# Performance work log

Measured on AMD Instinct MI355X. Metric: run time of the kernel, lower is better.

## Reference

```python
import jax, jax.numpy as jnp
import numpy as np

TAU = 1.0
MAX_ITER = 10


def setup_inputs() -> dict:
    key = jax.random.key(0)
    s = jax.random.normal(key, (32, 1024, 1024), dtype=jnp.float32)
    return {"s": s}


def reference(s) -> jnp.ndarray:
    # s: [B, N1, N2] with N1 <= N2 (square here), no padding -> fully vectorized
    log_s = s / TAU
    for i in range(MAX_ITER):
        # even iter: row normalization (logsumexp over columns, axis=2)
        # odd  iter: column normalization (logsumexp over rows, axis=1)
        axis = 2 if i % 2 == 0 else 1
        log_s = log_s - jax.nn.logsumexp(log_s, axis=axis, keepdims=True)
    return jnp.exp(log_s)
```

## Files before the change

### kernel.cpp

```cpp
#include <hip/hip_runtime.h>
#include <math.h>


#define BATCH 32
#define N 1024
#define RCHUNKS 32
#define ROWS_PER_BLK 32
#define BGROUPS 2
#define ROWS_PER_GROUP 16
#define PCHUNKS RCHUNKS

__global__ __launch_bounds__(512, 4) void fused_pair_kernel(
    const float* __restrict__ s, const float* __restrict__ c,
    float* __restrict__ r, float* __restrict__ pm, float* __restrict__ pl,
    int has_c)
{
    const int bc    = blockIdx.x;
    const int b     = bc >> 5;
    const int chunk = bc & 31;
    const int row0  = chunk * ROWS_PER_BLK;

    __shared__ float cs[N];
    __shared__ float rs[ROWS_PER_BLK];
    __shared__ float sm[BGROUPS][N];
    __shared__ float sl[BGROUPS][N];

    if (has_c) {
        ((float2*)cs)[threadIdx.x] = ((const float2*)(c + b * N))[threadIdx.x];
    } else {
        ((float2*)cs)[threadIdx.x] = make_float2(0.f, 0.f);
    }
    __syncthreads();

    const int wave = threadIdx.x >> 6;
    const int lane = threadIdx.x & 63;
    const float4* cs4 = (const float4*)cs;
#pragma unroll
    for (int rp = 0; rp < 4; rp++) {
        const int row = wave * 4 + rp;
        const float4* srow = (const float4*)(s + ((size_t)(b * N + row0 + row)) * N);
        float x[16];
#pragma unroll
        for (int k = 0; k < 4; k++) {
            float4 v  = srow[lane + 64 * k];
            float4 cv = cs4[lane + 64 * k];
            x[4*k+0] = v.x + cv.x; x[4*k+1] = v.y + cv.y;
            x[4*k+2] = v.z + cv.z; x[4*k+3] = v.w + cv.w;
        }
        float m = x[0];
#pragma unroll
        for (int t = 1; t < 16; t++) m = fmaxf(m, x[t]);
#pragma unroll
        for (int off = 32; off > 0; off >>= 1) m = fmaxf(m, __shfl_xor(m, off, 64));
        float sum = 0.f;
#pragma unroll
        for (int t = 0; t < 16; t++) sum += __expf(x[t] - m);
#pragma unroll
        for (int off = 32; off > 0; off >>= 1) sum += __shfl_xor(sum, off, 64);
        if (lane == 0) {
            float rv = -(m + __logf(sum));
            rs[row] = rv;
            r[b * N + row0 + row] = rv;
        }
    }
    __syncthreads();

    const int j4 = threadIdx.x & 255;
    const int g  = threadIdx.x >> 8;
    const float4* sb4 = (const float4*)(s + ((size_t)(b * N + row0 + g * ROWS_PER_GROUP)) * N);
    float m0=-3.0e38f, m1=-3.0e38f, m2=-3.0e38f, m3=-3.0e38f;
    float l0=0.f, l1=0.f, l2=0.f, l3=0.f;
#pragma unroll
    for (int i = 0; i < ROWS_PER_GROUP; i++) {
        float ri = rs[g * ROWS_PER_GROUP + i];
        float4 v = sb4[(size_t)i * 256 + j4];
        float x0 = v.x + ri, x1 = v.y + ri, x2 = v.z + ri, x3 = v.w + ri;
        float n0 = fmaxf(m0, x0); l0 = l0 * __expf(m0 - n0) + __expf(x0 - n0); m0 = n0;
        float n1 = fmaxf(m1, x1); l1 = l1 * __expf(m1 - n1) + __expf(x1 - n1); m1 = n1;
        float n2 = fmaxf(m2, x2); l2 = l2 * __expf(m2 - n2) + __expf(x2 - n2); m2 = n2;
        float n3 = fmaxf(m3, x3); l3 = l3 * __expf(m3 - n3) + __expf(x3 - n3); m3 = n3;
    }
    ((float4*)sm[g])[j4] = make_float4(m0, m1, m2, m3);
    ((float4*)sl[g])[j4] = make_float4(l0, l1, l2, l3);
    __syncthreads();

#pragma unroll
    for (int cc = 0; cc < 2; cc++) {
        const int col = threadIdx.x + cc * 512;
        float M = sm[0][col], L = sl[0][col];
        float m = sm[1][col], l = sl[1][col];
        float mn = fmaxf(M, m);
        L = L * __expf(M - mn) + l * __expf(m - mn);
        pm[(size_t)bc * N + col] = mn;
        pl[(size_t)bc * N + col] = L;
    }
}

__global__ __launch_bounds__(1024) void col_combine_kernel(
    const float* __restrict__ pm, const float* __restrict__ pl,
    float* __restrict__ c)
{
    const int b  = blockIdx.x >> 2;
    const int q  = blockIdx.x & 3;
    const int jc = threadIdx.x & 255;
    const int kg = threadIdx.x >> 8;
    const int j  = q * 256 + jc;
    float M = -3.0e38f, L = 0.f;
#pragma unroll
    for (int k = 0; k < 8; k++) {
        const int kk = kg * 8 + k;
        float m = pm[((size_t)(b * PCHUNKS + kk)) * N + j];
        float l = pl[((size_t)(b * PCHUNKS + kk)) * N + j];
        float mn = fmaxf(M, m);
        L = L * __expf(M - mn) + l * __expf(m - mn); M = mn;
    }
    __shared__ float smm[4][256], sll[4][256];
    smm[kg][jc] = M; sll[kg][jc] = L;
    __syncthreads();
    if (kg == 0) {
#pragma unroll
        for (int g2 = 1; g2 < 4; g2++) {
            float m = smm[g2][jc], l = sll[g2][jc];
            float mn = fmaxf(M, m);
            L = L * __expf(M - mn) + l * __expf(m - mn); M = mn;
        }
        c[b * N + j] = -(M + __logf(L));
    }
}

__global__ __launch_bounds__(256) void zero_c_kernel(float* __restrict__ c) {
    c[blockIdx.x * 256 + threadIdx.x] = 0.0f;
}

__global__ __launch_bounds__(256) void row_lse_kernel(const float* __restrict__ s,
                                                      const float* __restrict__ c,
                                                      float* __restrict__ r) {
    const int wave = threadIdx.x >> 6;
    const int lane = threadIdx.x & 63;
    const int row  = blockIdx.x * 4 + wave;
    const int b    = row >> 10;
    const float4* srow = (const float4*)(s + (size_t)row * N);
    const float4* crow = (const float4*)(c + (size_t)b * N);
    float x[16];
#pragma unroll
    for (int k = 0; k < 4; k++) {
        float4 v = srow[lane + k * 64];
        float4 cv = crow[lane + k * 64];
        x[4*k+0]=v.x+cv.x; x[4*k+1]=v.y+cv.y; x[4*k+2]=v.z+cv.z; x[4*k+3]=v.w+cv.w;
    }
    float m = x[0];
#pragma unroll
    for (int t = 1; t < 16; t++) m = fmaxf(m, x[t]);
#pragma unroll
    for (int off = 32; off > 0; off >>= 1) m = fmaxf(m, __shfl_xor(m, off, 64));
    float sum = 0.f;
#pragma unroll
    for (int t = 0; t < 16; t++) sum += __expf(x[t] - m);
#pragma unroll
    for (int off = 32; off > 0; off >>= 1) sum += __shfl_xor(sum, off, 64);
    if (lane == 0) r[row] = -(m + __logf(sum));
}

__global__ __launch_bounds__(1024) void col_lse_direct_kernel(const float* __restrict__ s,
                                                              const float* __restrict__ r,
                                                              float* __restrict__ c) {
    const int b = blockIdx.x;
    const int j = threadIdx.x;
    const float* rb = r + b * N;
    const float* base = s + (size_t)b * N * N + j;
    float m = -3.0e38f, l = 0.f;
    for (int i = 0; i < N; i++) {
        float x  = base[(size_t)i * N] + rb[i];
        float mn = fmaxf(m, x);
        l = l * __expf(m - mn) + __expf(x - mn);
        m = mn;
    }
    c[b * N + j] = -(m + __logf(l));
}

__global__ __launch_bounds__(256) void finalize_kernel(const float* __restrict__ s,
                                                       const float* __restrict__ r,
                                                       const float* __restrict__ c,
                                                       float* __restrict__ out) {
    const int f4  = blockIdx.x * 256 + threadIdx.x;
    const int j4  = f4 & 255;
    const int row = f4 >> 8;
    const int b   = row >> 10;
    float4 v  = ((const float4*)s)[f4];
    float  rr = r[row];
    float4 cc = ((const float4*)c)[(b << 8) + j4];
    float4 o;
    o.x = __expf(v.x + rr + cc.x);
    o.y = __expf(v.y + rr + cc.y);
    o.z = __expf(v.z + rr + cc.z);
    o.w = __expf(v.w + rr + cc.w);
    ((float4*)out)[f4] = o;
}

extern "C" void kernel_launch(void* const* d_in, const int* in_sizes, int n_in,
                              void* d_out, int out_size, void* d_ws, size_t ws_size,
                              hipStream_t stream) {
    const float* s = (const float*)d_in[0];
    float* out = (float*)d_out;

    float* c  = (float*)d_ws;
    float* r  = c + BATCH * N;
    float* pm = r + BATCH * N;
    float* pl = pm + BATCH * PCHUNKS * N;

    const size_t needed =
        (size_t)(2 * BATCH * N + 2 * BATCH * PCHUNKS * N) * sizeof(float);

    if (ws_size >= needed) {
        for (int p = 0; p < 5; p++) {
            fused_pair_kernel<<<BATCH * RCHUNKS, 512, 0, stream>>>(
                s, c, r, pm, pl, p > 0 ? 1 : 0);
            col_combine_kernel<<<BATCH * 4, 1024, 0, stream>>>(pm, pl, c);
        }
    } else {
        zero_c_kernel<<<(BATCH * N) / 256, 256, 0, stream>>>(c);
        for (int it = 0; it < 10; it++) {
            if ((it & 1) == 0)
                row_lse_kernel<<<(BATCH * N) / 4, 256, 0, stream>>>(s, c, r);
            else
                col_lse_direct_kernel<<<BATCH, 1024, 0, stream>>>(s, r, c);
        }
    }

    const int total_f4 = BATCH * N * N / 4;
    finalize_kernel<<<total_f4 / 256, 256, 0, stream>>>(s, r, c, out);
}
```

Baseline: 430.9 us.

## Keep row tiles in registers for column partials instead of reloading from global

The fused kernel now keeps the four rows each wave loads in registers and reuses them to compute per-wave column max/sum partials. Before, it re-read the 32-row tile from global memory in a second pass and ran a sequential online logsumexp. The eight per-wave partials are merged through shared memory, which removes a block barrier and half the global reads of s per pair. In exchange, register pressure rises (64 floats of x per thread, which could hurt occupancy at 512x4 launch bounds) and the shared-memory merge grows from 2 to 8 partials.

```diff
diff --git a/kernel.cpp b/kernel.cpp
--- a/kernel.cpp
+++ b/kernel.cpp
@@ -6,8 +6,6 @@
 #define N 1024
 #define RCHUNKS 32
 #define ROWS_PER_BLK 32
-#define BGROUPS 2
-#define ROWS_PER_GROUP 16
 #define PCHUNKS RCHUNKS
 
 __global__ __launch_bounds__(512, 4) void fused_pair_kernel(
@@ -19,79 +17,95 @@
     const int b     = bc >> 5;
     const int chunk = bc & 31;
     const int row0  = chunk * ROWS_PER_BLK;
-
-    __shared__ float cs[N];
-    __shared__ float rs[ROWS_PER_BLK];
-    __shared__ float sm[BGROUPS][N];
-    __shared__ float sl[BGROUPS][N];
-
+    const int wave  = threadIdx.x >> 6;
+    const int lane  = threadIdx.x & 63;
+
+    __shared__ float4 sm4[8][256];
+    __shared__ float4 sl4[8][256];
+
+    float4 cv[4];
     if (has_c) {
-        ((float2*)cs)[threadIdx.x] = ((const float2*)(c + b * N))[threadIdx.x];
+        const float4* c4 = (const float4*)(c + b * N);
+#pragma unroll
+        for (int k = 0; k < 4; k++) cv[k] = c4[lane + 64 * k];
     } else {
-        ((float2*)cs)[threadIdx.x] = make_float2(0.f, 0.f);
+#pragma unroll
+        for (int k = 0; k < 4; k++) cv[k] = make_float4(0.f, 0.f, 0.f, 0.f);
+    }
+
+    float x[4][16];
+#pragma unroll
+    for (int rp = 0; rp < 4; rp++) {
+        const float4* srow =
+            (const float4*)(s + ((size_t)(b * N + row0 + wave * 4 + rp)) * N);
+#pragma unroll
+        for (int k = 0; k < 4; k++) {
+            float4 v = srow[lane + 64 * k];
+            x[rp][4*k+0] = v.x + cv[k].x;
+            x[rp][4*k+1] = v.y + cv[k].y;
+            x[rp][4*k+2] = v.z + cv[k].z;
+            x[rp][4*k+3] = v.w + cv[k].w;
+        }
+    }
+
+    float rv[4];
+#pragma unroll
+    for (int rp = 0; rp < 4; rp++) {
+        float m = fmaxf(
+            fmaxf(fmaxf(fmaxf(x[rp][0],  x[rp][1]),  fmaxf(x[rp][2],  x[rp][3])),
+                  fmaxf(fmaxf(x[rp][4],  x[rp][5]),  fmaxf(x[rp][6],  x[rp][7]))),
+            fmaxf(fmaxf(fmaxf(x[rp][8],  x[rp][9]),  fmaxf(x[rp][10], x[rp][11])),
+                  fmaxf(fmaxf(x[rp][12], x[rp][13]), fmaxf(x[rp][14], x[rp][15]))));
+#pragma unroll
+        for (int off = 32; off > 0; off >>= 1) m = fmaxf(m, __shfl_xor(m, off, 64));
+        float s0 = 0.f, s1 = 0.f, s2 = 0.f, s3 = 0.f;
+#pragma unroll
+        for (int t = 0; t < 4; t++) {
+            s0 += __expf(x[rp][t]      - m);
+            s1 += __expf(x[rp][4 + t]  - m);
+            s2 += __expf(x[rp][8 + t]  - m);
+            s3 += __expf(x[rp][12 + t] - m);
+        }
+        float sum = (s0 + s1) + (s2 + s3);
+#pragma unroll
+        for (int off = 32; off > 0; off >>= 1) sum += __shfl_xor(sum, off, 64);
+        rv[rp] = -(m + __logf(sum));
+        if (lane == 0) r[b * N + row0 + wave * 4 + rp] = rv[rp];
+    }
+
+#pragma unroll
+    for (int k = 0; k < 4; k++) {
+        float pmv[4], plv[4];
+#pragma unroll
+        for (int e = 0; e < 4; e++) {
+            float x0 = x[0][4*k+e] + rv[0];
+            float x1 = x[1][4*k+e] + rv[1];
+            float x2 = x[2][4*k+e] + rv[2];
+            float x3 = x[3][4*k+e] + rv[3];
+            float m = fmaxf(fmaxf(x0, x1), fmaxf(x2, x3));
+            plv[e] = __expf(x0 - m) + __expf(x1 - m) +
+                     __expf(x2 - m) + __expf(x3 - m);
+            pmv[e] = m;
+        }
+        sm4[wave][lane + 64 * k] = make_float4(pmv[0], pmv[1], pmv[2], pmv[3]);
+        sl4[wave][lane + 64 * k] = make_float4(plv[0], plv[1], plv[2], plv[3]);
     }
     __syncthreads();
 
-    const int wave = threadIdx.x >> 6;
-    const int lane = threadIdx.x & 63;
-    const float4* cs4 = (const float4*)cs;
-#pragma unroll
-    for (int rp = 0; rp < 4; rp++) {
-        const int row = wave * 4 + rp;
-        const float4* srow = (const float4*)(s + ((size_t)(b * N + row0 + row)) * N);
-        float x[16];
-#pragma unroll
-        for (int k = 0; k < 4; k++) {
-            float4 v  = srow[lane + 64 * k];
-            float4 cv = cs4[lane + 64 * k];
-            x[4*k+0] = v.x + cv.x; x[4*k+1] = v.y + cv.y;
-            x[4*k+2] = v.z + cv.z; x[4*k+3] = v.w + cv.w;
-        }
-        float m = x[0];
-#pragma unroll
-        for (int t = 1; t < 16; t++) m = fmaxf(m, x[t]);
-#pragma unroll
-        for (int off = 32; off > 0; off >>= 1) m = fmaxf(m, __shfl_xor(m, off, 64));
-        float sum = 0.f;
-#pragma unroll
-        for (int t = 0; t < 16; t++) sum += __expf(x[t] - m);
-#pragma unroll
-        for (int off = 32; off > 0; off >>= 1) sum += __shfl_xor(sum, off, 64);
-        if (lane == 0) {
-            float rv = -(m + __logf(sum));
-            rs[row] = rv;
-            r[b * N + row0 + row] = rv;
-        }
-    }
-    __syncthreads();
-
-    const int j4 = threadIdx.x & 255;
-    const int g  = threadIdx.x >> 8;
-    const float4* sb4 = (const float4*)(s + ((size_t)(b * N + row0 + g * ROWS_PER_GROUP)) * N);
-    float m0=-3.0e38f, m1=-3.0e38f, m2=-3.0e38f, m3=-3.0e38f;
-    float l0=0.f, l1=0.f, l2=0.f, l3=0.f;
-#pragma unroll
-    for (int i = 0; i < ROWS_PER_GROUP; i++) {
-        float ri = rs[g * ROWS_PER_GROUP + i];
-        float4 v = sb4[(size_t)i * 256 + j4];
-        float x0 = v.x + ri, x1 = v.y + ri, x2 = v.z + ri, x3 = v.w + ri;
-        float n0 = fmaxf(m0, x0); l0 = l0 * __expf(m0 - n0) + __expf(x0 - n0); m0 = n0;
-        float n1 = fmaxf(m1, x1); l1 = l1 * __expf(m1 - n1) + __expf(x1 - n1); m1 = n1;
-        float n2 = fmaxf(m2, x2); l2 = l2 * __expf(m2 - n2) + __expf(x2 - n2); m2 = n2;
-        float n3 = fmaxf(m3, x3); l3 = l3 * __expf(m3 - n3) + __expf(x3 - n3); m3 = n3;
-    }
-    ((float4*)sm[g])[j4] = make_float4(m0, m1, m2, m3);
-    ((float4*)sl[g])[j4] = make_float4(l0, l1, l2, l3);
-    __syncthreads();
-
+    const float* smf = (const float*)sm4;
+    const float* slf = (const float*)sl4;
 #pragma unroll
     for (int cc = 0; cc < 2; cc++) {
         const int col = threadIdx.x + cc * 512;
-        float M = sm[0][col], L = sl[0][col];
-        float m = sm[1][col], l = sl[1][col];
-        float mn = fmaxf(M, m);
-        L = L * __expf(M - mn) + l * __expf(m - mn);
-        pm[(size_t)bc * N + col] = mn;
+        float M = smf[col], L = slf[col];
+#pragma unroll
+        for (int w = 1; w < 8; w++) {
+            float m = smf[w * N + col], l = slf[w * N + col];
+            float mn = fmaxf(M, m);
+            L = L * __expf(M - mn) + l * __expf(m - mn);
+            M = mn;
+        }
+        pm[(size_t)bc * N + col] = M;
         pl[(size_t)bc * N + col] = L;
     }
 }
```

New measurement: 373.1 us. 13.4% less time.
